# Optimization experiments

Measured on AMD Instinct MI355X. Metric: run time of the kernel, lower is better.

## Reference

```python
import jax, jax.numpy as jnp
import numpy as np


def setup_inputs() -> dict:
    key = jax.random.key(0)
    k = jax.random.split(key, 5)
    B, S, D, W = 8, 2048, 128, 16
    H4 = 4 * D
    scale = 1.0 / np.sqrt(D)
    return {
        "x": jax.random.normal(k[0], (B, S, D), dtype=jnp.float32),
        "w_ih": jax.random.uniform(k[1], (H4, D), jnp.float32, -scale, scale),
        "w_hh": jax.random.uniform(k[2], (H4, D), jnp.float32, -scale, scale),
        "b_ih": jax.random.uniform(k[3], (H4,), jnp.float32, -scale, scale),
        "b_hh": jax.random.uniform(k[4], (H4,), jnp.float32, -scale, scale),
        "window_size": W,
    }


def reference(x, w_ih, w_hh, b_ih, b_hh, window_size):
    # x: (B, S, D). Build overlapping causal windows of length W, run an LSTM
    # over each window independently, take the final hidden state per window.
    B, S, D = x.shape
    W = window_size
    pad = jnp.zeros((B, W - 1, D), dtype=x.dtype)
    xp = jnp.concatenate([pad, x], axis=1)                     # (B, S+W-1, D)
    idx = jnp.arange(S)[:, None] + jnp.arange(W)[None, :]      # (S, W)
    win = xp[:, idx]                                           # (B, S, W, D)
    xf = win.reshape(B * S, W, D)                              # (N, W, D), N=B*S
    # Precompute input-gate projections for all timesteps at once.
    xg = jnp.einsum('nwd,gd->nwg', xf, w_ih) + b_ih            # (N, W, 4D)

    def step(carry, gx):
        h, c = carry
        g = gx + h @ w_hh.T + b_hh                             # (N, 4D)
        i, f, gg, o = jnp.split(g, 4, axis=-1)                 # PyTorch gate order i,f,g,o
        c = jax.nn.sigmoid(f) * c + jax.nn.sigmoid(i) * jnp.tanh(gg)
        h = jax.nn.sigmoid(o) * jnp.tanh(c)
        return (h, c), None

    h0 = jnp.zeros((B * S, D), dtype=x.dtype)
    (h, _), _ = jax.lax.scan(step, (h0, h0), jnp.swapaxes(xg, 0, 1))
    return h.reshape(B, S, D)
```

## Files before the change

### kernel.cpp

```cpp
#include <hip/hip_runtime.h>

typedef __attribute__((ext_vector_type(8))) short bf16x8;
typedef __attribute__((ext_vector_type(4))) float f32x4;
typedef __attribute__((ext_vector_type(4))) _Float16 f16x4;
typedef __attribute__((ext_vector_type(2))) unsigned int u32x2;

#define B_N 8
#define S_N 2048
#define D_N 128
#define W_N 16
#define G_N 512
#define CH 64
#define ROWS 80

__device__ __forceinline__ short f2bf(float f) {
  union { float f; unsigned u; } v; v.f = f;
  unsigned r = v.u + 0x7fffu + ((v.u >> 16) & 1u);
  return (short)(r >> 16);
}

__device__ __forceinline__ bf16x8 cvt8(const float* p) {
  f32x4 a = *(const f32x4*)p;
  f32x4 b = *(const f32x4*)(p + 4);
  bf16x8 v;
  v[0] = f2bf(a[0]); v[1] = f2bf(a[1]); v[2] = f2bf(a[2]); v[3] = f2bf(a[3]);
  v[4] = f2bf(b[0]); v[5] = f2bf(b[1]); v[6] = f2bf(b[2]); v[7] = f2bf(b[3]);
  return v;
}

__device__ __forceinline__ float sigm(float x) {
  return __builtin_amdgcn_rcpf(1.0f + __builtin_amdgcn_exp2f(-1.4426950408889634f * x));
}
__device__ __forceinline__ float tanh_(float x) {
  return 2.0f * __builtin_amdgcn_rcpf(1.0f + __builtin_amdgcn_exp2f(-2.8853900817779268f * x)) - 1.0f;
}

__global__ void __launch_bounds__(512, 2)
fused_rnn(const float* __restrict__ x, const float* __restrict__ w_ih,
          const float* __restrict__ w_hh, const float* __restrict__ b_ih,
          const float* __restrict__ b_hh, float* __restrict__ out) {
  __shared__ char xg_s[ROWS * 1024];
  __shared__ char hbuf[2][CH * 256];

  const int tid  = threadIdx.x;
  const int lane = tid & 63;
  const int wv   = tid >> 6;
  const int lm   = lane & 15;
  const int q    = lane >> 4;
  const int n0   = blockIdx.x * CH;
  const int b    = n0 >> 11;
  const int s0   = n0 & (S_N - 1);

  bf16x8 wf[4][4];
#pragma unroll
  for (int i = 0; i < 4; ++i) {
    const int g = (wv + 8 * i) * 16 + lm;
#pragma unroll
    for (int kt = 0; kt < 4; ++kt)
      wf[i][kt] = cvt8(w_ih + g * D_N + kt * 32 + q * 8);
  }

  f32x4 bias[4];
#pragma unroll
  for (int i = 0; i < 4; ++i) {
    const int g0 = (wv + 8 * i) * 16 + 4 * q;
    f32x4 bi = *(const f32x4*)(b_ih + g0);
    f32x4 bh = *(const f32x4*)(b_hh + g0);
    bias[i].x = bi.x + bh.x; bias[i].y = bi.y + bh.y;
    bias[i].z = bi.z + bh.z; bias[i].w = bi.w + bh.w;
  }

#pragma unroll
  for (int rg = 0; rg < 5; ++rg) {
    const int r = rg * 16 + lm;
    const int t = s0 - (W_N - 1) + r;
    int tc = t < 0 ? 0 : t;
    tc = tc < S_N - 1 ? tc : S_N - 1;
    const bool valid = (t >= 0);
    const float* xr = x + ((long)b * S_N + tc) * D_N;
    bf16x8 xf[4];
#pragma unroll
    for (int kt = 0; kt < 4; ++kt) {
      if (valid) xf[kt] = cvt8(xr + kt * 32 + q * 8);
      else { bf16x8 z; for (int e = 0; e < 8; ++e) z[e] = 0; xf[kt] = z; }
    }
    f32x4 acc[4] = {{0,0,0,0},{0,0,0,0},{0,0,0,0},{0,0,0,0}};
#pragma unroll
    for (int i = 0; i < 4; ++i)
#pragma unroll
      for (int kt = 0; kt < 4; ++kt)
        acc[i] = __builtin_amdgcn_mfma_f32_16x16x32_bf16(wf[i][kt], xf[kt], acc[i], 0, 0, 0);
#pragma unroll
    for (int i = 0; i < 4; ++i) {
      const int g0 = (wv + 8 * i) * 16 + 4 * q;
      const int byte = (r * 1024 + g0 * 2) ^ ((r & 7) << 4);
      f16x4 hv;
      hv[0] = (_Float16)(acc[i][0] + bias[i].x);
      hv[1] = (_Float16)(acc[i][1] + bias[i].y);
      hv[2] = (_Float16)(acc[i][2] + bias[i].z);
      hv[3] = (_Float16)(acc[i][3] + bias[i].w);
      *(f16x4*)(xg_s + byte) = hv;
    }
  }

#pragma unroll
  for (int i = 0; i < 4; ++i) {
    const int g = (wv + 8 * i) * 16 + lm;
#pragma unroll
    for (int kt = 0; kt < 4; ++kt)
      wf[i][kt] = cvt8(w_hh + g * D_N + kt * 32 + q * 8);
  }
  __syncthreads();

  const int swz = (lm & 7) << 4;
  const int wrb = (lm * 256 + (16 * wv + 4 * q) * 2) ^ swz;
  int rdb[4];
#pragma unroll
  for (int kt = 0; kt < 4; ++kt)
    rdb[kt] = (lm * 256 + kt * 64 + q * 16) ^ swz;

  f32x4 c[4] = {{0,0,0,0},{0,0,0,0},{0,0,0,0},{0,0,0,0}};
  f32x4 hfin[4];

#pragma unroll
  for (int w = 0; w < W_N; ++w) {
#pragma unroll
    for (int cg = 0; cg < 4; ++cg) {
      const int row = cg * 16 + lm + w;
      f32x4 acc[4];
#pragma unroll
      for (int i = 0; i < 4; ++i) {
        const int g0 = (wv + 8 * i) * 16 + 4 * q;
        const int byte = (row * 1024 + g0 * 2) ^ ((row & 7) << 4);
        f16x4 xv = *(const f16x4*)(xg_s + byte);
        acc[i][0] = (float)xv[0]; acc[i][1] = (float)xv[1];
        acc[i][2] = (float)xv[2]; acc[i][3] = (float)xv[3];
      }

      if (w > 0) {
        const char* bb = hbuf[(w - 1) & 1] + cg * 4096;
        bf16x8 hf[4];
#pragma unroll
        for (int kt = 0; kt < 4; ++kt)
          hf[kt] = *(const bf16x8*)(bb + rdb[kt]);
#pragma unroll
        for (int i = 0; i < 4; ++i)
#pragma unroll
          for (int kt = 0; kt < 4; ++kt)
            acc[i] = __builtin_amdgcn_mfma_f32_16x16x32_bf16(wf[i][kt], hf[kt], acc[i], 0, 0, 0);
      }

      float hr[4];
#pragma unroll
      for (int r = 0; r < 4; ++r) {
        float cn = sigm(acc[1][r]) * c[cg][r] + sigm(acc[0][r]) * tanh_(acc[2][r]);
        c[cg][r] = cn;
        hr[r] = sigm(acc[3][r]) * tanh_(cn);
      }

      if (w < W_N - 1) {
        unsigned lo = ((unsigned)(unsigned short)f2bf(hr[0])) |
                      (((unsigned)(unsigned short)f2bf(hr[1])) << 16);
        unsigned hi = ((unsigned)(unsigned short)f2bf(hr[2])) |
                      (((unsigned)(unsigned short)f2bf(hr[3])) << 16);
        u32x2 v = {lo, hi};
        *(u32x2*)(&hbuf[w & 1][cg * 4096 + wrb]) = v;
      } else {
        hfin[cg][0] = hr[0]; hfin[cg][1] = hr[1];
        hfin[cg][2] = hr[2]; hfin[cg][3] = hr[3];
      }
    }
    __syncthreads();
  }

#pragma unroll
  for (int cg = 0; cg < 4; ++cg) {
    const int chain = cg * 16 + lm;
    const int byte = (chain * 512 + (16 * wv + 4 * q) * 4) ^ swz;
    *(f32x4*)(xg_s + byte) = hfin[cg];
  }
  __syncthreads();
#pragma unroll
  for (int p = 0; p < 4; ++p) {
    const int idx = p * 512 + tid;
    const int chain = idx >> 5;
    const int d4 = (idx & 31) * 4;
    const int byte = (chain * 512 + d4 * 4) ^ ((chain & 7) << 4);
    f32x4 v = *(const f32x4*)(xg_s + byte);
    *(f32x4*)(out + (long)(n0 + chain) * D_N + d4) = v;
  }
}

extern "C" void kernel_launch(void* const* d_in, const int* in_sizes, int n_in,
                              void* d_out, int out_size, void* d_ws, size_t ws_size,
                              hipStream_t stream) {
  const float* x    = (const float*)d_in[0];
  const float* w_ih = (const float*)d_in[1];
  const float* w_hh = (const float*)d_in[2];
  const float* b_ih = (const float*)d_in[3];
  const float* b_hh = (const float*)d_in[4];
  float* out = (float*)d_out;

  fused_rnn<<<(B_N * S_N) / CH, 512, 0, stream>>>(x, w_ih, w_hh, b_ih, b_hh, out);
}
```

Baseline: 144.9 us.

## Split chain groups across 16 waves and fuse LSTM gate reciprocals

Doubles the block to 1024 threads, with two wave halves each handling two of the four chain groups during the recurrence and splitting the input projection row groups. This shortens the per-wave serial loop per timestep. The gate nonlinearities are also combined algebraically so each element needs two reciprocals instead of five. The trade-offs are tighter register limits under the new launch bounds and possible overflow to inf/NaN for large pre-activations in the combined formula.

```diff
diff --git a/kernel.cpp b/kernel.cpp
--- a/kernel.cpp
+++ b/kernel.cpp
@@ -13,6 +13,9 @@
 #define CH 64
 #define ROWS 80
 
+#define L1 1.4426950408889634f
+#define L2 2.8853900817779268f
+
 __device__ __forceinline__ short f2bf(float f) {
   union { float f; unsigned u; } v; v.f = f;
   unsigned r = v.u + 0x7fffu + ((v.u >> 16) & 1u);
@@ -28,33 +31,28 @@
   return v;
 }
 
-__device__ __forceinline__ float sigm(float x) {
-  return __builtin_amdgcn_rcpf(1.0f + __builtin_amdgcn_exp2f(-1.4426950408889634f * x));
-}
-__device__ __forceinline__ float tanh_(float x) {
-  return 2.0f * __builtin_amdgcn_rcpf(1.0f + __builtin_amdgcn_exp2f(-2.8853900817779268f * x)) - 1.0f;
-}
-
-__global__ void __launch_bounds__(512, 2)
+__global__ void __launch_bounds__(1024, 4)
 fused_rnn(const float* __restrict__ x, const float* __restrict__ w_ih,
           const float* __restrict__ w_hh, const float* __restrict__ b_ih,
           const float* __restrict__ b_hh, float* __restrict__ out) {
   __shared__ char xg_s[ROWS * 1024];
   __shared__ char hbuf[2][CH * 256];
 
-  const int tid  = threadIdx.x;
-  const int lane = tid & 63;
-  const int wv   = tid >> 6;
-  const int lm   = lane & 15;
-  const int q    = lane >> 4;
-  const int n0   = blockIdx.x * CH;
-  const int b    = n0 >> 11;
-  const int s0   = n0 & (S_N - 1);
+  const int tid   = threadIdx.x;
+  const int lane  = tid & 63;
+  const int wv    = tid >> 6;
+  const int wv4   = wv & 7;
+  const int chalf = wv >> 3;
+  const int lm    = lane & 15;
+  const int q     = lane >> 4;
+  const int n0    = blockIdx.x * CH;
+  const int b     = n0 >> 11;
+  const int s0    = n0 & (S_N - 1);
 
   bf16x8 wf[4][4];
 #pragma unroll
   for (int i = 0; i < 4; ++i) {
-    const int g = (wv + 8 * i) * 16 + lm;
+    const int g = (wv4 + 8 * i) * 16 + lm;
 #pragma unroll
     for (int kt = 0; kt < 4; ++kt)
       wf[i][kt] = cvt8(w_ih + g * D_N + kt * 32 + q * 8);
@@ -63,49 +61,53 @@
   f32x4 bias[4];
 #pragma unroll
   for (int i = 0; i < 4; ++i) {
-    const int g0 = (wv + 8 * i) * 16 + 4 * q;
+    const int g0 = (wv4 + 8 * i) * 16 + 4 * q;
     f32x4 bi = *(const f32x4*)(b_ih + g0);
     f32x4 bh = *(const f32x4*)(b_hh + g0);
     bias[i].x = bi.x + bh.x; bias[i].y = bi.y + bh.y;
     bias[i].z = bi.z + bh.z; bias[i].w = bi.w + bh.w;
   }
 
-#pragma unroll
-  for (int rg = 0; rg < 5; ++rg) {
-    const int r = rg * 16 + lm;
-    const int t = s0 - (W_N - 1) + r;
-    int tc = t < 0 ? 0 : t;
-    tc = tc < S_N - 1 ? tc : S_N - 1;
-    const bool valid = (t >= 0);
-    const float* xr = x + ((long)b * S_N + tc) * D_N;
-    bf16x8 xf[4];
-#pragma unroll
-    for (int kt = 0; kt < 4; ++kt) {
-      if (valid) xf[kt] = cvt8(xr + kt * 32 + q * 8);
-      else { bf16x8 z; for (int e = 0; e < 8; ++e) z[e] = 0; xf[kt] = z; }
+  const int nrg = chalf ? 2 : 3;
+#pragma unroll
+  for (int rgi = 0; rgi < 3; ++rgi) {
+    if (rgi < nrg) {
+      const int rg = chalf ? 3 + rgi : rgi;
+      const int r = rg * 16 + lm;
+      const int t = s0 - (W_N - 1) + r;
+      int tc = t < 0 ? 0 : t;
+      tc = tc < S_N - 1 ? tc : S_N - 1;
+      const bool valid = (t >= 0);
+      const float* xr = x + ((long)b * S_N + tc) * D_N;
+      bf16x8 xf[4];
+#pragma unroll
+      for (int kt = 0; kt < 4; ++kt) {
+        if (valid) xf[kt] = cvt8(xr + kt * 32 + q * 8);
+        else { bf16x8 z; for (int e = 0; e < 8; ++e) z[e] = 0; xf[kt] = z; }
+      }
+      f32x4 acc[4] = {{0,0,0,0},{0,0,0,0},{0,0,0,0},{0,0,0,0}};
+#pragma unroll
+      for (int i = 0; i < 4; ++i)
+#pragma unroll
+        for (int kt = 0; kt < 4; ++kt)
+          acc[i] = __builtin_amdgcn_mfma_f32_16x16x32_bf16(wf[i][kt], xf[kt], acc[i], 0, 0, 0);
+#pragma unroll
+      for (int i = 0; i < 4; ++i) {
+        const int g0 = (wv4 + 8 * i) * 16 + 4 * q;
+        const int byte = (r * 1024 + g0 * 2) ^ ((r & 7) << 4);
+        f16x4 hv;
+        hv[0] = (_Float16)(acc[i][0] + bias[i].x);
+        hv[1] = (_Float16)(acc[i][1] + bias[i].y);
+        hv[2] = (_Float16)(acc[i][2] + bias[i].z);
+        hv[3] = (_Float16)(acc[i][3] + bias[i].w);
+        *(f16x4*)(xg_s + byte) = hv;
+      }
     }
-    f32x4 acc[4] = {{0,0,0,0},{0,0,0,0},{0,0,0,0},{0,0,0,0}};
-#pragma unroll
-    for (int i = 0; i < 4; ++i)
-#pragma unroll
-      for (int kt = 0; kt < 4; ++kt)
-        acc[i] = __builtin_amdgcn_mfma_f32_16x16x32_bf16(wf[i][kt], xf[kt], acc[i], 0, 0, 0);
-#pragma unroll
-    for (int i = 0; i < 4; ++i) {
-      const int g0 = (wv + 8 * i) * 16 + 4 * q;
-      const int byte = (r * 1024 + g0 * 2) ^ ((r & 7) << 4);
-      f16x4 hv;
-      hv[0] = (_Float16)(acc[i][0] + bias[i].x);
-      hv[1] = (_Float16)(acc[i][1] + bias[i].y);
-      hv[2] = (_Float16)(acc[i][2] + bias[i].z);
-      hv[3] = (_Float16)(acc[i][3] + bias[i].w);
-      *(f16x4*)(xg_s + byte) = hv;
-    }
   }
 
 #pragma unroll
   for (int i = 0; i < 4; ++i) {
-    const int g = (wv + 8 * i) * 16 + lm;
+    const int g = (wv4 + 8 * i) * 16 + lm;
 #pragma unroll
     for (int kt = 0; kt < 4; ++kt)
       wf[i][kt] = cvt8(w_hh + g * D_N + kt * 32 + q * 8);
@@ -113,24 +115,25 @@
   __syncthreads();
 
   const int swz = (lm & 7) << 4;
-  const int wrb = (lm * 256 + (16 * wv + 4 * q) * 2) ^ swz;
+  const int wrb = (lm * 256 + (16 * wv4 + 4 * q) * 2) ^ swz;
   int rdb[4];
 #pragma unroll
   for (int kt = 0; kt < 4; ++kt)
     rdb[kt] = (lm * 256 + kt * 64 + q * 16) ^ swz;
 
-  f32x4 c[4] = {{0,0,0,0},{0,0,0,0},{0,0,0,0},{0,0,0,0}};
-  f32x4 hfin[4];
+  f32x4 c[2] = {{0,0,0,0},{0,0,0,0}};
+  f32x4 hfin[2];
 
 #pragma unroll
   for (int w = 0; w < W_N; ++w) {
 #pragma unroll
-    for (int cg = 0; cg < 4; ++cg) {
+    for (int cg2 = 0; cg2 < 2; ++cg2) {
+      const int cg = 2 * chalf + cg2;
       const int row = cg * 16 + lm + w;
       f32x4 acc[4];
 #pragma unroll
       for (int i = 0; i < 4; ++i) {
-        const int g0 = (wv + 8 * i) * 16 + 4 * q;
+        const int g0 = (wv4 + 8 * i) * 16 + 4 * q;
         const int byte = (row * 1024 + g0 * 2) ^ ((row & 7) << 4);
         f16x4 xv = *(const f16x4*)(xg_s + byte);
         acc[i][0] = (float)xv[0]; acc[i][1] = (float)xv[1];
@@ -153,9 +156,17 @@
       float hr[4];
 #pragma unroll
       for (int r = 0; r < 4; ++r) {
-        float cn = sigm(acc[1][r]) * c[cg][r] + sigm(acc[0][r]) * tanh_(acc[2][r]);
-        c[cg][r] = cn;
-        hr[r] = sigm(acc[3][r]) * tanh_(cn);
+        float ei = __builtin_amdgcn_exp2f(-L1 * acc[0][r]);
+        float ef = __builtin_amdgcn_exp2f(-L1 * acc[1][r]);
+        float eg = __builtin_amdgcn_exp2f(-L2 * acc[2][r]);
+        float a   = (1.0f + ei) * (1.0f + eg);
+        float num = c[cg2][r] * a + (1.0f - eg) * (1.0f + ef);
+        float den = (1.0f + ef) * a;
+        float cn  = num * __builtin_amdgcn_rcpf(den);
+        c[cg2][r] = cn;
+        float eo = __builtin_amdgcn_exp2f(-L1 * acc[3][r]);
+        float ec = __builtin_amdgcn_exp2f(-L2 * cn);
+        hr[r] = (1.0f - ec) * __builtin_amdgcn_rcpf((1.0f + eo) * (1.0f + ec));
       }
 
       if (w < W_N - 1) {
@@ -166,23 +177,23 @@
         u32x2 v = {lo, hi};
         *(u32x2*)(&hbuf[w & 1][cg * 4096 + wrb]) = v;
       } else {
-        hfin[cg][0] = hr[0]; hfin[cg][1] = hr[1];
-        hfin[cg][2] = hr[2]; hfin[cg][3] = hr[3];
+        hfin[cg2][0] = hr[0]; hfin[cg2][1] = hr[1];
+        hfin[cg2][2] = hr[2]; hfin[cg2][3] = hr[3];
       }
     }
     __syncthreads();
   }
 
 #pragma unroll
-  for (int cg = 0; cg < 4; ++cg) {
-    const int chain = cg * 16 + lm;
-    const int byte = (chain * 512 + (16 * wv + 4 * q) * 4) ^ swz;
-    *(f32x4*)(xg_s + byte) = hfin[cg];
+  for (int cg2 = 0; cg2 < 2; ++cg2) {
+    const int chain = (2 * chalf + cg2) * 16 + lm;
+    const int byte = (chain * 512 + (16 * wv4 + 4 * q) * 4) ^ swz;
+    *(f32x4*)(xg_s + byte) = hfin[cg2];
   }
   __syncthreads();
 #pragma unroll
-  for (int p = 0; p < 4; ++p) {
-    const int idx = p * 512 + tid;
+  for (int p = 0; p < 2; ++p) {
+    const int idx = p * 1024 + tid;
     const int chain = idx >> 5;
     const int d4 = (idx & 31) * 4;
     const int byte = (chain * 512 + d4 * 4) ^ ((chain & 7) << 4);
@@ -201,5 +212,5 @@
   const float* b_hh = (const float*)d_in[4];
   float* out = (float*)d_out;
 
-  fused_rnn<<<(B_N * S_N) / CH, 512, 0, stream>>>(x, w_ih, w_hh, b_ih, b_hh, out);
-}
+  fused_rnn<<<(B_N * S_N) / CH, 1024, 0, stream>>>(x, w_ih, w_hh, b_ih, b_hh, out);
+}
```

After: 256.7 us. +77.1%, slower.

## Halve chains per block, merge LSTM gate divides, write bf16 final state

Applied to the files above, without the earlier changes.

Reduces chains per block from 64 to 32, which doubles the grid and shrinks LDS use so more blocks can be resident. The input projection now recomputes 48 rows per 32 chains instead of 80 per 64, so more of that work is redundant. The gate math merges sigmoid and tanh reciprocals into shared rcp calls, and the final hidden state is taken from the bf16 LDS buffer rather than kept in fp32. That loses precision in the output, and the merged products could overflow for large pre-activations.

```diff
diff --git a/kernel.cpp b/kernel.cpp
--- a/kernel.cpp
+++ b/kernel.cpp
@@ -10,8 +10,11 @@
 #define D_N 128
 #define W_N 16
 #define G_N 512
-#define CH 64
-#define ROWS 80
+#define CH 32
+#define ROWS 48
+
+#define L1 1.4426950408889634f
+#define L2 2.8853900817779268f
 
 __device__ __forceinline__ short f2bf(float f) {
   union { float f; unsigned u; } v; v.f = f;
@@ -26,13 +29,6 @@
   v[0] = f2bf(a[0]); v[1] = f2bf(a[1]); v[2] = f2bf(a[2]); v[3] = f2bf(a[3]);
   v[4] = f2bf(b[0]); v[5] = f2bf(b[1]); v[6] = f2bf(b[2]); v[7] = f2bf(b[3]);
   return v;
-}
-
-__device__ __forceinline__ float sigm(float x) {
-  return __builtin_amdgcn_rcpf(1.0f + __builtin_amdgcn_exp2f(-1.4426950408889634f * x));
-}
-__device__ __forceinline__ float tanh_(float x) {
-  return 2.0f * __builtin_amdgcn_rcpf(1.0f + __builtin_amdgcn_exp2f(-2.8853900817779268f * x)) - 1.0f;
 }
 
 __global__ void __launch_bounds__(512, 2)
@@ -60,46 +56,48 @@
       wf[i][kt] = cvt8(w_ih + g * D_N + kt * 32 + q * 8);
   }
 
-  f32x4 bias[4];
-#pragma unroll
-  for (int i = 0; i < 4; ++i) {
-    const int g0 = (wv + 8 * i) * 16 + 4 * q;
-    f32x4 bi = *(const f32x4*)(b_ih + g0);
-    f32x4 bh = *(const f32x4*)(b_hh + g0);
-    bias[i].x = bi.x + bh.x; bias[i].y = bi.y + bh.y;
-    bias[i].z = bi.z + bh.z; bias[i].w = bi.w + bh.w;
-  }
-
-#pragma unroll
-  for (int rg = 0; rg < 5; ++rg) {
-    const int r = rg * 16 + lm;
-    const int t = s0 - (W_N - 1) + r;
-    int tc = t < 0 ? 0 : t;
-    tc = tc < S_N - 1 ? tc : S_N - 1;
-    const bool valid = (t >= 0);
-    const float* xr = x + ((long)b * S_N + tc) * D_N;
-    bf16x8 xf[4];
-#pragma unroll
-    for (int kt = 0; kt < 4; ++kt) {
-      if (valid) xf[kt] = cvt8(xr + kt * 32 + q * 8);
-      else { bf16x8 z; for (int e = 0; e < 8; ++e) z[e] = 0; xf[kt] = z; }
-    }
-    f32x4 acc[4] = {{0,0,0,0},{0,0,0,0},{0,0,0,0},{0,0,0,0}};
-#pragma unroll
-    for (int i = 0; i < 4; ++i)
-#pragma unroll
-      for (int kt = 0; kt < 4; ++kt)
-        acc[i] = __builtin_amdgcn_mfma_f32_16x16x32_bf16(wf[i][kt], xf[kt], acc[i], 0, 0, 0);
+  {
+    f32x4 bias[4];
 #pragma unroll
     for (int i = 0; i < 4; ++i) {
       const int g0 = (wv + 8 * i) * 16 + 4 * q;
-      const int byte = (r * 1024 + g0 * 2) ^ ((r & 7) << 4);
-      f16x4 hv;
-      hv[0] = (_Float16)(acc[i][0] + bias[i].x);
-      hv[1] = (_Float16)(acc[i][1] + bias[i].y);
-      hv[2] = (_Float16)(acc[i][2] + bias[i].z);
-      hv[3] = (_Float16)(acc[i][3] + bias[i].w);
-      *(f16x4*)(xg_s + byte) = hv;
+      f32x4 bi = *(const f32x4*)(b_ih + g0);
+      f32x4 bh = *(const f32x4*)(b_hh + g0);
+      bias[i].x = bi.x + bh.x; bias[i].y = bi.y + bh.y;
+      bias[i].z = bi.z + bh.z; bias[i].w = bi.w + bh.w;
+    }
+
+#pragma unroll
+    for (int rg = 0; rg < 3; ++rg) {
+      const int r = rg * 16 + lm;
+      const int t = s0 - (W_N - 1) + r;
+      int tc = t < 0 ? 0 : t;
+      tc = tc < S_N - 1 ? tc : S_N - 1;
+      const bool valid = (t >= 0);
+      const float* xr = x + ((long)b * S_N + tc) * D_N;
+      bf16x8 xf[4];
+#pragma unroll
+      for (int kt = 0; kt < 4; ++kt) {
+        if (valid) xf[kt] = cvt8(xr + kt * 32 + q * 8);
+        else { bf16x8 z; for (int e = 0; e < 8; ++e) z[e] = 0; xf[kt] = z; }
+      }
+      f32x4 acc[4] = {{0,0,0,0},{0,0,0,0},{0,0,0,0},{0,0,0,0}};
+#pragma unroll
+      for (int i = 0; i < 4; ++i)
+#pragma unroll
+        for (int kt = 0; kt < 4; ++kt)
+          acc[i] = __builtin_amdgcn_mfma_f32_16x16x32_bf16(wf[i][kt], xf[kt], acc[i], 0, 0, 0);
+#pragma unroll
+      for (int i = 0; i < 4; ++i) {
+        const int g0 = (wv + 8 * i) * 16 + 4 * q;
+        const int byte = (r * 1024 + g0 * 2) ^ ((r & 7) << 4);
+        f16x4 hv;
+        hv[0] = (_Float16)(acc[i][0] + bias[i].x);
+        hv[1] = (_Float16)(acc[i][1] + bias[i].y);
+        hv[2] = (_Float16)(acc[i][2] + bias[i].z);
+        hv[3] = (_Float16)(acc[i][3] + bias[i].w);
+        *(f16x4*)(xg_s + byte) = hv;
+      }
     }
   }
 
@@ -119,13 +117,12 @@
   for (int kt = 0; kt < 4; ++kt)
     rdb[kt] = (lm * 256 + kt * 64 + q * 16) ^ swz;
 
-  f32x4 c[4] = {{0,0,0,0},{0,0,0,0},{0,0,0,0},{0,0,0,0}};
-  f32x4 hfin[4];
+  f32x4 c[2] = {{0,0,0,0},{0,0,0,0}};
 
 #pragma unroll
   for (int w = 0; w < W_N; ++w) {
 #pragma unroll
-    for (int cg = 0; cg < 4; ++cg) {
+    for (int cg = 0; cg < 2; ++cg) {
       const int row = cg * 16 + lm + w;
       f32x4 acc[4];
 #pragma unroll
@@ -139,55 +136,60 @@
 
       if (w > 0) {
         const char* bb = hbuf[(w - 1) & 1] + cg * 4096;
-        bf16x8 hf[4];
-#pragma unroll
-        for (int kt = 0; kt < 4; ++kt)
-          hf[kt] = *(const bf16x8*)(bb + rdb[kt]);
-#pragma unroll
-        for (int i = 0; i < 4; ++i)
-#pragma unroll
-          for (int kt = 0; kt < 4; ++kt)
-            acc[i] = __builtin_amdgcn_mfma_f32_16x16x32_bf16(wf[i][kt], hf[kt], acc[i], 0, 0, 0);
+#pragma unroll
+        for (int kh = 0; kh < 2; ++kh) {
+          bf16x8 hf0 = *(const bf16x8*)(bb + rdb[2 * kh]);
+          bf16x8 hf1 = *(const bf16x8*)(bb + rdb[2 * kh + 1]);
+#pragma unroll
+          for (int i = 0; i < 4; ++i) {
+            acc[i] = __builtin_amdgcn_mfma_f32_16x16x32_bf16(wf[i][2 * kh],     hf0, acc[i], 0, 0, 0);
+            acc[i] = __builtin_amdgcn_mfma_f32_16x16x32_bf16(wf[i][2 * kh + 1], hf1, acc[i], 0, 0, 0);
+          }
+        }
       }
 
       float hr[4];
 #pragma unroll
       for (int r = 0; r < 4; ++r) {
-        float cn = sigm(acc[1][r]) * c[cg][r] + sigm(acc[0][r]) * tanh_(acc[2][r]);
+        float ei = __builtin_amdgcn_exp2f(-L1 * acc[0][r]);
+        float ef = __builtin_amdgcn_exp2f(-L1 * acc[1][r]);
+        float eg = __builtin_amdgcn_exp2f(-L2 * acc[2][r]);
+        float a   = (1.0f + ei) * (1.0f + eg);
+        float num = c[cg][r] * a + (1.0f - eg) * (1.0f + ef);
+        float den = (1.0f + ef) * a;
+        float cn  = num * __builtin_amdgcn_rcpf(den);
         c[cg][r] = cn;
-        hr[r] = sigm(acc[3][r]) * tanh_(cn);
-      }
-
-      if (w < W_N - 1) {
-        unsigned lo = ((unsigned)(unsigned short)f2bf(hr[0])) |
-                      (((unsigned)(unsigned short)f2bf(hr[1])) << 16);
-        unsigned hi = ((unsigned)(unsigned short)f2bf(hr[2])) |
-                      (((unsigned)(unsigned short)f2bf(hr[3])) << 16);
-        u32x2 v = {lo, hi};
-        *(u32x2*)(&hbuf[w & 1][cg * 4096 + wrb]) = v;
-      } else {
-        hfin[cg][0] = hr[0]; hfin[cg][1] = hr[1];
-        hfin[cg][2] = hr[2]; hfin[cg][3] = hr[3];
-      }
+        float eo = __builtin_amdgcn_exp2f(-L1 * acc[3][r]);
+        float ec = __builtin_amdgcn_exp2f(-L2 * cn);
+        hr[r] = (1.0f - ec) * __builtin_amdgcn_rcpf((1.0f + eo) * (1.0f + ec));
+      }
+
+      unsigned lo = ((unsigned)(unsigned short)f2bf(hr[0])) |
+                    (((unsigned)(unsigned short)f2bf(hr[1])) << 16);
+      unsigned hi = ((unsigned)(unsigned short)f2bf(hr[2])) |
+                    (((unsigned)(unsigned short)f2bf(hr[3])) << 16);
+      u32x2 v = {lo, hi};
+      *(u32x2*)(&hbuf[w & 1][cg * 4096 + wrb]) = v;
     }
     __syncthreads();
   }
 
-#pragma unroll
-  for (int cg = 0; cg < 4; ++cg) {
-    const int chain = cg * 16 + lm;
-    const int byte = (chain * 512 + (16 * wv + 4 * q) * 4) ^ swz;
-    *(f32x4*)(xg_s + byte) = hfin[cg];
-  }
-  __syncthreads();
-#pragma unroll
-  for (int p = 0; p < 4; ++p) {
-    const int idx = p * 512 + tid;
-    const int chain = idx >> 5;
-    const int d4 = (idx & 31) * 4;
-    const int byte = (chain * 512 + d4 * 4) ^ ((chain & 7) << 4);
-    f32x4 v = *(const f32x4*)(xg_s + byte);
-    *(f32x4*)(out + (long)(n0 + chain) * D_N + d4) = v;
+  {
+    const int chain = tid >> 4;
+    const int d0 = (tid & 15) * 8;
+    const int byte = (chain * 256 + d0 * 2) ^ ((chain & 7) << 4);
+    bf16x8 hv = *(const bf16x8*)(&hbuf[1][byte]);
+    float* op = out + (long)(n0 + chain) * D_N + d0;
+    f32x4 v0, v1;
+#pragma unroll
+    for (int e = 0; e < 4; ++e) {
+      union { unsigned u; float f; } t0, t1;
+      t0.u = ((unsigned)(unsigned short)hv[e]) << 16;
+      t1.u = ((unsigned)(unsigned short)hv[4 + e]) << 16;
+      v0[e] = t0.f; v1[e] = t1.f;
+    }
+    *(f32x4*)op = v0;
+    *(f32x4*)(op + 4) = v1;
   }
 }
 
```

After: 157.2 us. 1.08x slower.
